# Performance work log

Measured on AMD Instinct MI355X. Metric: run time of the kernel, lower is better.

The kernel has to match this reference:

```python
import jax, jax.numpy as jnp
import numpy as np
import math

M = 4096   # mem_dim == hidden_size (required: C @ qt)
D = 2048   # input_size


def setup_inputs() -> dict:
    key = jax.random.key(0)
    ks = jax.random.split(key, 16)
    f = lambda k, s: jax.random.normal(k, s, dtype=jnp.float32)
    return {
        "x": f(ks[0], (D, 1)),
        "cp": f(ks[1], (M, M)),
        "n_prev": f(ks[2], (M, 1)),
        "Wq": f(ks[3], (M, D)),
        "bq": f(ks[4], (M, 1)),
        "Wk": f(ks[5], (M, D)),
        "bk": f(ks[6], (M, 1)),
        "Wv": f(ks[7], (M, D)),
        "bV": f(ks[8], (M, 1)),
        "Wi": f(ks[9], (1, D)),
        "bi": f(ks[10], (1,)),
        "Wf": f(ks[11], (1, D)),
        "bf": f(ks[12], (1,)),
        "Wo": f(ks[13], (1, D)),
        "bo": f(ks[14], (1,)),
    }


def reference(x, cp, n_prev, Wq, bq, Wk, bk, Wv, bV, Wi, bi, Wf, bf, Wo, bo):
    inv_sqrt_m = 1.0 / math.sqrt(M)
    qt = Wq @ x + bq                      # (M, 1)
    kt = inv_sqrt_m * (Wk @ x + bk)       # (M, 1)
    vt = Wv @ x + bV                      # (M, 1)
    it = jnp.exp(Wi @ x + bi)             # (1, 1) input gate (exp)
    ft = jnp.exp(Wf @ x + bf)             # (1, 1) forget gate (exp)
    v = vt[:, 0]                          # (M,)
    k = kt[:, 0]                          # (M,)
    # matrix memory update: C = f*C_prev + i * v k^T
    C = ft * cp + it * jnp.outer(v, k)    # (M, M)
    n = ft * n_prev + it * k[:, None]     # (M, 1)
    denom = jnp.maximum(jnp.abs(n.T @ qt), 1.0)   # (1, 1)
    h_tilde = (C @ qt) / denom            # (M, 1)
    ot = jax.nn.sigmoid(Wo @ x + bo)      # (1, 1)
    ht = ot * h_tilde                     # (M, 1)
    return (ht, C, n)
```

## Files before the change

kernel.cpp:

```cpp
#include <hip/hip_runtime.h>
#include <math.h>

#define MM 4096
#define DD 2048
#define CHUNK 1024

typedef float floatx4 __attribute__((ext_vector_type(4)));


__device__ __forceinline__ void async_copy_1k(const float* src, float* lds_dst, int lane)
{
    __builtin_amdgcn_global_load_lds(
        (const __attribute__((address_space(1))) void*)(src + lane * 4),
        (__attribute__((address_space(3))) void*)lds_dst,
        16, 0, 0);
}

__global__ __launch_bounds__(256) void k1_gemv_gates(
    const float* __restrict__ x,
    const float* __restrict__ Wq, const float* __restrict__ bq,
    const float* __restrict__ Wk, const float* __restrict__ bk,
    const float* __restrict__ Wv, const float* __restrict__ bV,
    const float* __restrict__ Wi, const float* __restrict__ bi,
    const float* __restrict__ Wf, const float* __restrict__ bf,
    const float* __restrict__ Wo, const float* __restrict__ bo,
    float* __restrict__ ws)
{
    const int lane = threadIdx.x & 63;
    const int wid  = threadIdx.x >> 6;

    if (blockIdx.x >= 1024) {
        __shared__ double gred[4];
        const int g = blockIdx.x - 1024;
        const float* G = (g == 0) ? Wi : ((g == 1) ? Wf : Wo);
        const float4* g4 = (const float4*)G;
        const float4* xv = (const float4*)x;
        double acc = 0.0;
        for (int t = threadIdx.x; t < DD / 4; t += 256) {
            float4 gg = g4[t];
            float4 xx = xv[t];
            acc += (double)gg.x * xx.x + (double)gg.y * xx.y
                 + (double)gg.z * xx.z + (double)gg.w * xx.w;
        }
        for (int off = 32; off; off >>= 1) acc += __shfl_down(acc, off, 64);
        if (lane == 0) gred[wid] = acc;
        __syncthreads();
        if (threadIdx.x == 0) {
            double s = gred[0] + gred[1] + gred[2] + gred[3];
            if (g == 0)      ws[3 * MM + 0] = (float)exp(s + (double)bi[0]);
            else if (g == 1) ws[3 * MM + 1] = (float)exp(s + (double)bf[0]);
            else             ws[3 * MM + 2] = (float)(1.0 / (1.0 + exp(-(s + (double)bo[0]))));
        }
        return;
    }

    __shared__ float xs[DD];
    __shared__ float wbuf[4][3][CHUNK];

    {
        const float4* xv  = (const float4*)x;
        float4*       xsv = (float4*)xs;
        xsv[threadIdx.x]       = xv[threadIdx.x];
        xsv[256 + threadIdx.x] = xv[256 + threadIdx.x];
    }

    const int row = blockIdx.x * 4 + wid;
    const float* wqrow = Wq + (size_t)row * DD;
    const float* wkrow = Wk + (size_t)row * DD;
    const float* wvrow = Wv + (size_t)row * DD;

    float aq = 0.f, ak = 0.f, av = 0.f;

    #pragma unroll
    for (int h = 0; h < DD / CHUNK; ++h) {
        #pragma unroll
        for (int c = 0; c < CHUNK / 256; ++c) {
            async_copy_1k(wqrow + h * CHUNK + c * 256, &wbuf[wid][0][c * 256], lane);
            async_copy_1k(wkrow + h * CHUNK + c * 256, &wbuf[wid][1][c * 256], lane);
            async_copy_1k(wvrow + h * CHUNK + c * 256, &wbuf[wid][2][c * 256], lane);
        }
        __syncthreads();

        const float4* xs4 = (const float4*)(xs + h * CHUNK);
        const float4* q4  = (const float4*)wbuf[wid][0];
        const float4* k4  = (const float4*)wbuf[wid][1];
        const float4* v4  = (const float4*)wbuf[wid][2];
        #pragma unroll
        for (int t = 0; t < CHUNK / 4 / 64; ++t) {
            float4 xx = xs4[lane + 64 * t];
            float4 qq = q4 [lane + 64 * t];
            float4 kk = k4 [lane + 64 * t];
            float4 vv = v4 [lane + 64 * t];
            aq += qq.x * xx.x + qq.y * xx.y + qq.z * xx.z + qq.w * xx.w;
            ak += kk.x * xx.x + kk.y * xx.y + kk.z * xx.z + kk.w * xx.w;
            av += vv.x * xx.x + vv.y * xx.y + vv.z * xx.z + vv.w * xx.w;
        }
        __syncthreads();
    }

    for (int off = 32; off; off >>= 1) {
        aq += __shfl_down(aq, off, 64);
        ak += __shfl_down(ak, off, 64);
        av += __shfl_down(av, off, 64);
    }
    if (lane == 0) {
        ws[row]          = aq + bq[row];
        ws[MM + row]     = (ak + bk[row]) * (1.0f / 64.0f);
        ws[2 * MM + row] = av + bV[row];
    }
}

__global__ __launch_bounds__(256) void k2_rowC(
    const float* __restrict__ cp, const float* __restrict__ n_prev,
    float* __restrict__ ws, float* __restrict__ C_out, float* __restrict__ n_out)
{
    const int lane = threadIdx.x & 63;
    const int wid  = threadIdx.x >> 6;

    if (blockIdx.x == MM) {
        __shared__ float pred[4];
        const float it = ws[3 * MM + 0];
        const float ft = ws[3 * MM + 1];
        const float4* np4 = (const float4*)n_prev;
        const float4* kv4 = (const float4*)(ws + MM);
        const float4* qv4 = (const float4*)ws;
        float4* n4 = (float4*)n_out;
        float acc = 0.f;
        #pragma unroll
        for (int u = 0; u < 4; ++u) {
            int t = threadIdx.x + 256 * u;
            float4 np = np4[t], kk = kv4[t], qq = qv4[t];
            float4 nn;
            nn.x = fmaf(ft, np.x, it * kk.x);
            nn.y = fmaf(ft, np.y, it * kk.y);
            nn.z = fmaf(ft, np.z, it * kk.z);
            nn.w = fmaf(ft, np.w, it * kk.w);
            n4[t] = nn;
            acc += nn.x * qq.x + nn.y * qq.y + nn.z * qq.z + nn.w * qq.w;
        }
        for (int off = 32; off; off >>= 1) acc += __shfl_down(acc, off, 64);
        if (lane == 0) pred[wid] = acc;
        __syncthreads();
        if (threadIdx.x == 0) {
            float s = pred[0] + pred[1] + pred[2] + pred[3];
            ws[3 * MM + 3] = fmaxf(fabsf(s), 1.0f);
        }
        return;
    }

    __shared__ float sred[4];
    const int row = blockIdx.x;
    const float it  = ws[3 * MM + 0];
    const float ft  = ws[3 * MM + 1];
    const float ivi = it * ws[2 * MM + row];

    const float4* cprow = (const float4*)(cp + (size_t)row * MM);
    const float4* kv4   = (const float4*)(ws + MM);
    const float4* qv4   = (const float4*)ws;
    float4*       crow  = (float4*)(C_out + (size_t)row * MM);

    float4 c[4], kk[4], qq[4];
    #pragma unroll
    for (int u = 0; u < 4; ++u) c[u]  = cprow[threadIdx.x + 256 * u];
    #pragma unroll
    for (int u = 0; u < 4; ++u) kk[u] = kv4[threadIdx.x + 256 * u];
    #pragma unroll
    for (int u = 0; u < 4; ++u) qq[u] = qv4[threadIdx.x + 256 * u];

    float acc = 0.f;
    #pragma unroll
    for (int u = 0; u < 4; ++u) {
        float4 o;
        o.x = fmaf(ivi, kk[u].x, ft * c[u].x);
        o.y = fmaf(ivi, kk[u].y, ft * c[u].y);
        o.z = fmaf(ivi, kk[u].z, ft * c[u].z);
        o.w = fmaf(ivi, kk[u].w, ft * c[u].w);
        floatx4 ov = { o.x, o.y, o.z, o.w };
        __builtin_nontemporal_store(ov, (floatx4*)(crow + threadIdx.x + 256 * u));
        acc += o.x * qq[u].x + o.y * qq[u].y + o.z * qq[u].z + o.w * qq[u].w;
    }
    for (int off = 32; off; off >>= 1) acc += __shfl_down(acc, off, 64);
    if (lane == 0) sred[wid] = acc;
    __syncthreads();
    if (threadIdx.x == 0)
        ws[4 * MM + row] = sred[0] + sred[1] + sred[2] + sred[3];
}

__global__ __launch_bounds__(256) void k3_finalize(
    const float* __restrict__ ws, float* __restrict__ ht_out)
{
    const float ot    = ws[3 * MM + 2];
    const float denom = ws[3 * MM + 3];
    const int i = blockIdx.x * 256 + threadIdx.x;
    ht_out[i] = ot * (ws[4 * MM + i] / denom);
}

extern "C" void kernel_launch(void* const* d_in, const int* in_sizes, int n_in,
                              void* d_out, int out_size, void* d_ws, size_t ws_size,
                              hipStream_t stream)
{
    const float* x      = (const float*)d_in[0];
    const float* cp     = (const float*)d_in[1];
    const float* n_prev = (const float*)d_in[2];
    const float* Wq = (const float*)d_in[3];
    const float* bq = (const float*)d_in[4];
    const float* Wk = (const float*)d_in[5];
    const float* bk = (const float*)d_in[6];
    const float* Wv = (const float*)d_in[7];
    const float* bV = (const float*)d_in[8];
    const float* Wi = (const float*)d_in[9];
    const float* bi = (const float*)d_in[10];
    const float* Wf = (const float*)d_in[11];
    const float* bf = (const float*)d_in[12];
    const float* Wo = (const float*)d_in[13];
    const float* bo = (const float*)d_in[14];

    float* out = (float*)d_out;
    float* ht  = out;
    float* C   = out + MM;
    float* n   = out + MM + (size_t)MM * MM;
    float* ws  = (float*)d_ws;

    k1_gemv_gates<<<1027, 256, 0, stream>>>(x, Wq, bq, Wk, bk, Wv, bV,
                                            Wi, bi, Wf, bf, Wo, bo, ws);
    k2_rowC      <<<MM + 1, 256, 0, stream>>>(cp, n_prev, ws, C, n);
    k3_finalize  <<<MM / 256, 256, 0, stream>>>(ws, ht);
}
```

Measured before the change: 225.7 us.

## Split QKV GEMV across separate blocks and load weights directly to registers

The GEMV kernel now launches three times as many blocks, one set per weight matrix (Wq, Wk, Wv), so each wave computes a single row dot product. It drops the async global-to-LDS staging buffer and its barriers and reads weights straight into registers with float4 loads. The goal is more parallelism and more bytes in flight, plus higher occupancy from the much smaller LDS footprint. In exchange each block reloads x into LDS, and a per-wave register load loop may expose more memory latency than the batched async copies did.

Result: no change. 223.8 us (-0.9%).

```diff
diff --git a/kernel.cpp b/kernel.cpp
--- a/kernel.cpp
+++ b/kernel.cpp
@@ -3,18 +3,9 @@
 
 #define MM 4096
 #define DD 2048
-#define CHUNK 1024
 
 typedef float floatx4 __attribute__((ext_vector_type(4)));
 
-
-__device__ __forceinline__ void async_copy_1k(const float* src, float* lds_dst, int lane)
-{
-    __builtin_amdgcn_global_load_lds(
-        (const __attribute__((address_space(1))) void*)(src + lane * 4),
-        (__attribute__((address_space(3))) void*)lds_dst,
-        16, 0, 0);
-}
 
 __global__ __launch_bounds__(256) void k1_gemv_gates(
     const float* __restrict__ x,
@@ -29,9 +20,9 @@
     const int lane = threadIdx.x & 63;
     const int wid  = threadIdx.x >> 6;
 
-    if (blockIdx.x >= 1024) {
+    if (blockIdx.x >= 3072) {
         __shared__ double gred[4];
-        const int g = blockIdx.x - 1024;
+        const int g = blockIdx.x - 3072;
         const float* G = (g == 0) ? Wi : ((g == 1) ? Wf : Wo);
         const float4* g4 = (const float4*)G;
         const float4* xv = (const float4*)x;
@@ -55,7 +46,6 @@
     }
 
     __shared__ float xs[DD];
-    __shared__ float wbuf[4][3][CHUNK];
 
     {
         const float4* xv  = (const float4*)x;
@@ -63,50 +53,29 @@
         xsv[threadIdx.x]       = xv[threadIdx.x];
         xsv[256 + threadIdx.x] = xv[256 + threadIdx.x];
     }
+    __syncthreads();
 
-    const int row = blockIdx.x * 4 + wid;
-    const float* wqrow = Wq + (size_t)row * DD;
-    const float* wkrow = Wk + (size_t)row * DD;
-    const float* wvrow = Wv + (size_t)row * DD;
+    const int m   = blockIdx.x >> 10;
+    const int row = ((blockIdx.x & 1023) << 2) + wid;
 
-    float aq = 0.f, ak = 0.f, av = 0.f;
+    const float* W = (m == 0) ? Wq : ((m == 1) ? Wk : Wv);
+    const float4* w4  = (const float4*)(W + (size_t)row * DD);
+    const float4* xs4 = (const float4*)xs;
 
+    float acc = 0.f;
     #pragma unroll
-    for (int h = 0; h < DD / CHUNK; ++h) {
-        #pragma unroll
-        for (int c = 0; c < CHUNK / 256; ++c) {
-            async_copy_1k(wqrow + h * CHUNK + c * 256, &wbuf[wid][0][c * 256], lane);
-            async_copy_1k(wkrow + h * CHUNK + c * 256, &wbuf[wid][1][c * 256], lane);
-            async_copy_1k(wvrow + h * CHUNK + c * 256, &wbuf[wid][2][c * 256], lane);
-        }
-        __syncthreads();
-
-        const float4* xs4 = (const float4*)(xs + h * CHUNK);
-        const float4* q4  = (const float4*)wbuf[wid][0];
-        const float4* k4  = (const float4*)wbuf[wid][1];
-        const float4* v4  = (const float4*)wbuf[wid][2];
-        #pragma unroll
-        for (int t = 0; t < CHUNK / 4 / 64; ++t) {
-            float4 xx = xs4[lane + 64 * t];
-            float4 qq = q4 [lane + 64 * t];
-            float4 kk = k4 [lane + 64 * t];
-            float4 vv = v4 [lane + 64 * t];
-            aq += qq.x * xx.x + qq.y * xx.y + qq.z * xx.z + qq.w * xx.w;
-            ak += kk.x * xx.x + kk.y * xx.y + kk.z * xx.z + kk.w * xx.w;
-            av += vv.x * xx.x + vv.y * xx.y + vv.z * xx.z + vv.w * xx.w;
-        }
-        __syncthreads();
+    for (int t = 0; t < DD / 4 / 64; ++t) {
+        float4 ww = w4 [t * 64 + lane];
+        float4 xx = xs4[t * 64 + lane];
+        acc += ww.x * xx.x + ww.y * xx.y + ww.z * xx.z + ww.w * xx.w;
     }
 
-    for (int off = 32; off; off >>= 1) {
-        aq += __shfl_down(aq, off, 64);
-        ak += __shfl_down(ak, off, 64);
-        av += __shfl_down(av, off, 64);
-    }
+    for (int off = 32; off; off >>= 1) acc += __shfl_down(acc, off, 64);
+
     if (lane == 0) {
-        ws[row]          = aq + bq[row];
-        ws[MM + row]     = (ak + bk[row]) * (1.0f / 64.0f);
-        ws[2 * MM + row] = av + bV[row];
+        if (m == 0)      ws[row]          = acc + bq[row];
+        else if (m == 1) ws[MM + row]     = (acc + bk[row]) * (1.0f / 64.0f);
+        else             ws[2 * MM + row] = acc + bV[row];
     }
 }
 
@@ -221,7 +190,7 @@
     float* n   = out + MM + (size_t)MM * MM;
     float* ws  = (float*)d_ws;
 
-    k1_gemv_gates<<<1027, 256, 0, stream>>>(x, Wq, bq, Wk, bk, Wv, bV,
+    k1_gemv_gates<<<3075, 256, 0, stream>>>(x, Wq, bq, Wk, bk, Wv, bV,
                                             Wi, bi, Wf, bf, Wo, bo, ws);
     k2_rowC      <<<MM + 1, 256, 0, stream>>>(cp, n_prev, ws, C, n);
     k3_finalize  <<<MM / 256, 256, 0, stream>>>(ws, ht);
```
